# Optimization experiments

Hardware: AMD Instinct MI355X
Metric: run time of the kernel (lower is better)

The kernel has to match this reference:

```python
import jax, jax.numpy as jnp
import numpy as np

DIM, HEADS = 1024, 16
HEAD_DIM = DIM // HEADS
SCALE = HEAD_DIM ** -0.5


def setup_inputs() -> dict:
    key = jax.random.key(0)
    ks = jax.random.split(key, 5)
    B, N = 2, 2048
    x = jax.random.normal(ks[0], (B, N, DIM), dtype=jnp.float32)
    freqs = jax.random.normal(ks[1], (N, HEAD_DIM // 2), dtype=jnp.float32)
    w_qkv = jax.random.normal(ks[2], (3 * DIM, DIM), dtype=jnp.float32) * 0.02
    w_proj = jax.random.normal(ks[3], (DIM, DIM), dtype=jnp.float32) * 0.02
    b_proj = jnp.zeros((DIM,), dtype=jnp.float32)
    return {"x": x, "freqs": freqs, "w_qkv": w_qkv, "w_proj": w_proj, "b_proj": b_proj}


def _apply_rotary(t, cos, sin):
    # t: (B,N,H,D); cos/sin: (1,N,1,D//2)
    B, N, H, D = t.shape
    tp = t.reshape(B, N, H, D // 2, 2)
    x1, x2 = tp[..., 0], tp[..., 1]
    out = jnp.stack([x1 * cos - x2 * sin, x1 * sin + x2 * cos], axis=-1)
    return out.reshape(B, N, H, D)


def reference(x, freqs, w_qkv, w_proj, b_proj):
    B, N, C = x.shape
    H, D = HEADS, HEAD_DIM
    qkv = (x @ w_qkv.T).reshape(B, N, 3, H, D)  # fused QKV projection
    q, k, v = qkv[:, :, 0], qkv[:, :, 1], qkv[:, :, 2]  # each (B,N,H,D)
    cos = jnp.cos(freqs)[None, :, None, :]  # (1,N,1,D/2)
    sin = jnp.sin(freqs)[None, :, None, :]
    q = _apply_rotary(q, cos, sin)
    k = _apply_rotary(k, cos, sin)
    # SDPA: scores (B,H,N,N)
    scores = jnp.einsum("bqhd,bkhd->bhqk", q, k) * SCALE
    attn = jax.nn.softmax(scores, axis=-1)
    out = jnp.einsum("bhqk,bkhd->bqhd", attn, v).reshape(B, N, C)
    return out @ w_proj.T + b_proj
```

## Files before the change

### kernel.cpp

```cpp
#include <hip/hip_runtime.h>
#include <hip/hip_bf16.h>
#include <stdint.h>

#define BATCH   2
#define SEQ     2048
#define CDIM    1024
#define NHEAD   16
#define HDIM    64
#define MROWS   (BATCH*SEQ)
#define QKVN    (3*CDIM)
#define QSCALE  0.18033688011112042f

typedef __hip_bfloat16 bf16;
using bf16x8 = __attribute__((ext_vector_type(8))) __bf16;
using f32x4  = __attribute__((ext_vector_type(4))) float;
using s16x4  = __attribute__((ext_vector_type(4))) short;

__device__ __forceinline__ void gld16(const void* g, void* l) {
    __builtin_amdgcn_global_load_lds(
        (__attribute__((address_space(1))) void*)(void*)(g),
        (__attribute__((address_space(3))) void*)(l),
        16, 0, 0);
}

__device__ __forceinline__ f32x4 mfma16x16x32(bf16x8 a, bf16x8 b, f32x4 c) {
    return __builtin_amdgcn_mfma_f32_16x16x32_bf16(a, b, c, 0, 0, 0);
}
__device__ __forceinline__ f32x4 mfma16x16x16(s16x4 a, s16x4 b, f32x4 c) {
    return __builtin_amdgcn_mfma_f32_16x16x16bf16_1k(a, b, c, 0, 0, 0);
}

__device__ __forceinline__ uint16_t bfbits(float v) {
    bf16 b = __float2bfloat16(v);
    return *(uint16_t*)&b;
}
__device__ __forceinline__ uint32_t pkbf(float a, float b) {
    uint32_t au = __builtin_bit_cast(uint32_t, a);
    uint32_t bu = __builtin_bit_cast(uint32_t, b);
    return ((au + 0x8000u) >> 16) | ((bu + 0x8000u) & 0xffff0000u);
}

#define NX_F4 ((size_t)MROWS*CDIM/4)
#define NQ_F4 ((size_t)QKVN*CDIM/4)
#define NP_F4 ((size_t)CDIM*CDIM/4)
#define NF_SC ((size_t)SEQ*32)

__global__ __launch_bounds__(256)
void cvt_kernel(const float* __restrict__ x, const float* __restrict__ wq,
                const float* __restrict__ wp, const float* __restrict__ freqs,
                bf16* __restrict__ xb, bf16* __restrict__ wqb,
                bf16* __restrict__ wpb, float2* __restrict__ csn) {
    size_t i4 = (size_t)blockIdx.x*256 + threadIdx.x;
    if (i4 < NX_F4 + NQ_F4 + NP_F4) {
        const float* src; bf16* dst; size_t off;
        if (i4 < NX_F4)           { src = x;  dst = xb;  off = i4; }
        else if (i4 < NX_F4+NQ_F4){ src = wq; dst = wqb; off = i4 - NX_F4; }
        else                      { src = wp; dst = wpb; off = i4 - NX_F4 - NQ_F4; }
        float4 v = ((const float4*)src)[off];
        bf16 o[4] = { __float2bfloat16(v.x), __float2bfloat16(v.y),
                      __float2bfloat16(v.z), __float2bfloat16(v.w) };
        *(uint64_t*)(dst + off*4) = *(const uint64_t*)o;
    } else if (i4 < NX_F4 + NQ_F4 + NP_F4 + NF_SC) {
        size_t k = i4 - (NX_F4 + NQ_F4 + NP_F4);
        float f = freqs[k];
        csn[k] = make_float2(cosf(f), sinf(f));
    }
}

__global__ __launch_bounds__(256)
void gemm_qkv_rope(const bf16* __restrict__ A, const bf16* __restrict__ Bw,
                   const float2* __restrict__ csn, bf16* __restrict__ Qr,
                   bf16* __restrict__ Kr, bf16* __restrict__ VG) {
    const int K = CDIM;
    __shared__ __align__(16) bf16 As[128*32];
    __shared__ __align__(16) bf16 Bs[128*32];

    const int bm = blockIdx.x, bn = blockIdx.y;
    const int tid  = threadIdx.x;
    const int lane = tid & 63;
    const int w    = tid >> 6;
    const int wm   = (w & 1) * 64;
    const int wn   = (w >> 1) * 64;
    const int quad = lane >> 4;
    const int l16  = lane & 15;

    const int c0 = tid, c1 = tid + 256;
    const size_t a_off0 = (size_t)(bm*128 + (c0 >> 2)) * K + (c0 & 3) * 8;
    const size_t a_off1 = (size_t)(bm*128 + (c1 >> 2)) * K + (c1 & 3) * 8;
    const size_t b_off0 = (size_t)(bn*128 + (c0 >> 2)) * K + (c0 & 3) * 8;
    const size_t b_off1 = (size_t)(bn*128 + (c1 >> 2)) * K + (c1 & 3) * 8;

    f32x4 acc[4][4] = {};

    for (int k0 = 0; k0 < K; k0 += 32) {
        __syncthreads();
        gld16(A + a_off0 + k0, &As[c0*8]);
        gld16(A + a_off1 + k0, &As[c1*8]);
        gld16(Bw + b_off0 + k0, &Bs[c0*8]);
        gld16(Bw + b_off1 + k0, &Bs[c1*8]);
        __syncthreads();

        bf16x8 af[4], bfv[4];
#pragma unroll
        for (int i = 0; i < 4; i++)
            af[i] = *(const bf16x8*)&As[(wm + i*16 + l16)*32 + quad*8];
#pragma unroll
        for (int i = 0; i < 4; i++)
            bfv[i] = *(const bf16x8*)&Bs[(wn + i*16 + l16)*32 + quad*8];
#pragma unroll
        for (int mi = 0; mi < 4; mi++)
#pragma unroll
            for (int ni = 0; ni < 4; ni++)
                acc[mi][ni] = mfma16x16x32(af[mi], bfv[ni], acc[mi][ni]);
    }

    const int region = bn >> 3;
    if (region < 2) {
        bf16* dst = region ? Kr : Qr;
        const float qs = region ? 1.0f : QSCALE;
        const int odd = l16 & 1;
#pragma unroll
        for (int mi = 0; mi < 4; mi++) {
#pragma unroll
            for (int ni = 0; ni < 4; ni++) {
                const int cq = (bn & 7)*128 + wn + ni*16 + l16;
                const int h = cq >> 6, d = cq & 63, fi = d >> 1;
#pragma unroll
                for (int r = 0; r < 4; r++) {
                    const int m = bm*128 + wm + mi*16 + quad*4 + r;
                    const int bb = m >> 11, n = m & 2047;
                    float own = acc[mi][ni][r];
                    float prt = __shfl_xor(own, 1);
                    float2 cs2 = csn[n*32 + fi];
                    float o = odd ? (prt*cs2.y + own*cs2.x)
                                  : (own*cs2.x - prt*cs2.y);
                    dst[((size_t)(bb*16 + h)*SEQ + n)*HDIM + d] =
                        __float2bfloat16(o * qs);
                }
            }
        }
    } else {
        const int bb  = (bm*128) >> 11, n0l = (bm*128) & 2047;
        const int h   = (bn - 16)*2 + (wn >> 6);
        bf16* vg = VG + (size_t)(bb*16 + h) * (SEQ*HDIM);
#pragma unroll
        for (int mi = 0; mi < 4; mi++) {
            const int tile = (n0l >> 6) + ((wm + mi*16) >> 6);
            const int j    = ((wm + mi*16) >> 4) & 3;
#pragma unroll
            for (int ni = 0; ni < 4; ni++) {
                uint2 pk;
                pk.x = (uint32_t)bfbits(acc[mi][ni][0]) |
                       ((uint32_t)bfbits(acc[mi][ni][1]) << 16);
                pk.y = (uint32_t)bfbits(acc[mi][ni][2]) |
                       ((uint32_t)bfbits(acc[mi][ni][3]) << 16);
                const int slot = (j*4 + ni)*64 + quad*16 + l16;
                *(uint2*)&vg[(size_t)tile*4096 + slot*4] = pk;
            }
        }
    }
}

__global__ __launch_bounds__(256)
void gemm_proj(const bf16* __restrict__ A, const bf16* __restrict__ Bw,
               const float* __restrict__ bias, float* __restrict__ C,
               int M, int N, int K) {
    __shared__ __align__(16) bf16 As[64*32];
    __shared__ __align__(16) bf16 Bs[128*32];

    const int bm = blockIdx.x, bn = blockIdx.y;
    const int tid  = threadIdx.x;
    const int lane = tid & 63;
    const int w    = tid >> 6;
    const int wm   = (w & 1) * 32;
    const int wn   = (w >> 1) * 64;
    const int quad = lane >> 4;
    const int l16  = lane & 15;

    const int ca = tid, cb0 = tid, cb1 = tid + 256;
    const size_t a_off  = (size_t)(bm*64  + (ca  >> 2)) * K + (ca  & 3) * 8;
    const size_t b_off0 = (size_t)(bn*128 + (cb0 >> 2)) * K + (cb0 & 3) * 8;
    const size_t b_off1 = (size_t)(bn*128 + (cb1 >> 2)) * K + (cb1 & 3) * 8;

    f32x4 acc[2][4] = {};

    for (int k0 = 0; k0 < K; k0 += 32) {
        __syncthreads();
        gld16(A + a_off + k0, &As[ca*8]);
        gld16(Bw + b_off0 + k0, &Bs[cb0*8]);
        gld16(Bw + b_off1 + k0, &Bs[cb1*8]);
        __syncthreads();

        bf16x8 af[2], bfv[4];
#pragma unroll
        for (int i = 0; i < 2; i++)
            af[i] = *(const bf16x8*)&As[(wm + i*16 + l16)*32 + quad*8];
#pragma unroll
        for (int i = 0; i < 4; i++)
            bfv[i] = *(const bf16x8*)&Bs[(wn + i*16 + l16)*32 + quad*8];
#pragma unroll
        for (int mi = 0; mi < 2; mi++)
#pragma unroll
            for (int ni = 0; ni < 4; ni++)
                acc[mi][ni] = mfma16x16x32(af[mi], bfv[ni], acc[mi][ni]);
    }

#pragma unroll
    for (int mi = 0; mi < 2; mi++) {
        const int r0 = bm*64 + wm + mi*16 + quad*4;
#pragma unroll
        for (int ni = 0; ni < 4; ni++) {
            const int c = bn*128 + wn + ni*16 + l16;
            const float bv = bias[c];
#pragma unroll
            for (int r = 0; r < 4; r++)
                C[(size_t)(r0 + r)*N + c] = acc[mi][ni][r] + bv;
        }
    }
}

__global__ __launch_bounds__(64)
void attn_kernel(const bf16* __restrict__ Qr, const bf16* __restrict__ Kr,
                 const bf16* __restrict__ VG, bf16* __restrict__ Ao) {
    const int blk = blockIdx.x;
    const int bh  = blk >> 5;
    const int b   = bh >> 4, h = bh & 15;
    const int q0  = (blk & 31) * 64;
    const int lane = threadIdx.x;
    const int quad = lane >> 4, l16 = lane & 15;
    const int swz  = l16 & 7;

    __shared__ __align__(16) bf16 Ks[2][64*64];
    __shared__ __align__(16) bf16 Vs[2][64*64];

    bf16x8 qf[4][2];
#pragma unroll
    for (int t = 0; t < 4; t++) {
        const int qrow = q0 + t*16 + l16;
        const bf16* qp = Qr + ((size_t)bh*SEQ + qrow)*HDIM + quad*8;
        qf[t][0] = *(const bf16x8*)(qp);
        qf[t][1] = *(const bf16x8*)(qp + 32);
    }

    const bf16* KrB = Kr + (size_t)bh*SEQ*HDIM;
    const bf16* VgB = VG + (size_t)bh*SEQ*HDIM;
    int koff[8];
#pragma unroll
    for (int k = 0; k < 8; k++) {
        int c = lane + 64*k;
        int r = c >> 3, g = (c & 7) ^ (r & 7);
        koff[k] = r*HDIM + g*8;
    }

    f32x4 acc[4][4] = {};
    float lsum[4] = {};

#pragma unroll
    for (int k = 0; k < 8; k++) {
        gld16(KrB + koff[k], &Ks[0][(lane + 64*k)*8]);
        gld16(VgB + (lane + 64*k)*8, &Vs[0][(lane + 64*k)*8]);
    }

    for (int it = 0; it < SEQ/64; ++it) {
        const int cur = it & 1, nxt = cur ^ 1;
        bf16x8 kfr[4][2];
#pragma unroll
        for (int j = 0; j < 4; j++) {
            const bf16* krow = &Ks[cur][(j*16 + l16)*64];
            kfr[j][0] = *(const bf16x8*)(krow + ((quad     ^ swz) * 8));
            kfr[j][1] = *(const bf16x8*)(krow + (((quad+4) ^ swz) * 8));
        }
        s16x4 vfr[16];
#pragma unroll
        for (int m = 0; m < 16; m++)
            vfr[m] = *(const s16x4*)&Vs[cur][(m*64 + lane)*4];

        if (it + 1 < SEQ/64) {
            const size_t o = (size_t)(it + 1) * 4096;
#pragma unroll
            for (int k = 0; k < 8; k++) {
                gld16(KrB + koff[k] + o, &Ks[nxt][(lane + 64*k)*8]);
                gld16(VgB + (lane + 64*k)*8 + o, &Vs[nxt][(lane + 64*k)*8]);
            }
        }

        s16x4 pf[4][4];
#pragma unroll
        for (int j = 0; j < 4; j++) {
#pragma unroll
            for (int t = 0; t < 4; t++) {
                f32x4 sv = {};
                sv = mfma16x16x32(kfr[j][0], qf[t][0], sv);
                sv = mfma16x16x32(kfr[j][1], qf[t][1], sv);
                float e0 = __builtin_amdgcn_exp2f(sv[0]);
                float e1 = __builtin_amdgcn_exp2f(sv[1]);
                float e2 = __builtin_amdgcn_exp2f(sv[2]);
                float e3 = __builtin_amdgcn_exp2f(sv[3]);
                lsum[t] += (e0 + e1) + (e2 + e3);
                union { uint32_t u[2]; s16x4 v; } pa;
                pa.u[0] = pkbf(e0, e1);
                pa.u[1] = pkbf(e2, e3);
                pf[t][j] = pa.v;
            }
        }

#pragma unroll
        for (int dt = 0; dt < 4; dt++) {
#pragma unroll
            for (int j = 0; j < 4; j++) {
                s16x4 vf = vfr[j*4 + dt];
#pragma unroll
                for (int t = 0; t < 4; t++)
                    acc[t][dt] = mfma16x16x16(pf[t][j], vf, acc[t][dt]);
            }
        }
    }

#pragma unroll
    for (int t = 0; t < 4; t++) {
        lsum[t] += __shfl_xor(lsum[t], 16, 64);
        lsum[t] += __shfl_xor(lsum[t], 32, 64);
    }
    float lt[4][4];
#pragma unroll
    for (int t = 0; t < 4; t++)
#pragma unroll
        for (int r = 0; r < 4; r++)
            lt[t][r] = __shfl(lsum[t], quad*20 + r, 64);

#pragma unroll
    for (int t = 0; t < 4; t++)
#pragma unroll
        for (int dt = 0; dt < 4; dt++)
#pragma unroll
            for (int r = 0; r < 4; r++) {
                int qr  = q0 + t*16 + quad*4 + r;
                int col = h*HDIM + dt*16 + l16;
                Ao[(size_t)(b*SEQ + qr)*CDIM + col] =
                    __float2bfloat16(acc[t][dt][r] / lt[t][r]);
            }
}

extern "C" void kernel_launch(void* const* d_in, const int* in_sizes, int n_in,
                              void* d_out, int out_size, void* d_ws, size_t ws_size,
                              hipStream_t stream) {
    const float* x      = (const float*)d_in[0];
    const float* freqs  = (const float*)d_in[1];
    const float* w_qkv  = (const float*)d_in[2];
    const float* w_proj = (const float*)d_in[3];
    const float* b_proj = (const float*)d_in[4];
    float* out = (float*)d_out;

    char* ws = (char*)d_ws;
    bf16*   xb    = (bf16*)ws;   ws += (size_t)MROWS * CDIM * sizeof(bf16);
    bf16*   wqkvb = (bf16*)ws;   ws += (size_t)QKVN * CDIM * sizeof(bf16);
    bf16*   wprojb= (bf16*)ws;   ws += (size_t)CDIM * CDIM * sizeof(bf16);
    float2* csn   = (float2*)ws; ws += (size_t)SEQ * 32 * sizeof(float2);
    bf16*   Qr    = (bf16*)ws;   ws += (size_t)BATCH*NHEAD*SEQ*HDIM*sizeof(bf16);
    bf16*   Kr    = (bf16*)ws;   ws += (size_t)BATCH*NHEAD*SEQ*HDIM*sizeof(bf16);
    bf16*   VG    = (bf16*)ws;   ws += (size_t)BATCH*NHEAD*SEQ*HDIM*sizeof(bf16);
    bf16*   Ao    = (bf16*)ws;

    {
        size_t nthr = NX_F4 + NQ_F4 + NP_F4 + NF_SC;
        cvt_kernel<<<dim3((nthr + 255) / 256), dim3(256), 0, stream>>>(
            x, w_qkv, w_proj, freqs, xb, wqkvb, wprojb, csn);
    }
    gemm_qkv_rope<<<dim3(MROWS/128, QKVN/128), dim3(256), 0, stream>>>(
        xb, wqkvb, csn, Qr, Kr, VG);
    attn_kernel<<<dim3(BATCH*NHEAD*(SEQ/64)), dim3(64), 0, stream>>>(
        Qr, Kr, VG, Ao);
    gemm_proj<<<dim3(MROWS/64, CDIM/128), dim3(256), 0, stream>>>(
        Ao, wprojb, b_proj, out, MROWS, CDIM, CDIM);
}
```

Measured before the change: 208.3 us.

## Share K/V LDS tiles across four waves per attention block

The attention kernel now runs 256-thread blocks that cover 256 queries instead of 64-thread blocks that cover 64. The four waves load each K/V tile together and share it in LDS, so each tile is fetched from global memory or L2 four times less often. The prefetch of the next tile moves to the top of the loop behind a __syncthreads, which adds a block-wide barrier every iteration. The grid shrinks to a quarter as many blocks, which lowers the scheduler's flexibility in spreading work across CUs.

New measurement: 215.0 us. 3.2% more time.

```diff
diff --git a/kernel.cpp b/kernel.cpp
--- a/kernel.cpp
+++ b/kernel.cpp
@@ -219,14 +219,15 @@
     }
 }
 
-__global__ __launch_bounds__(64)
+__global__ __launch_bounds__(256)
 void attn_kernel(const bf16* __restrict__ Qr, const bf16* __restrict__ Kr,
                  const bf16* __restrict__ VG, bf16* __restrict__ Ao) {
     const int blk = blockIdx.x;
-    const int bh  = blk >> 5;
+    const int bh  = blk >> 3;
     const int b   = bh >> 4, h = bh & 15;
-    const int q0  = (blk & 31) * 64;
-    const int lane = threadIdx.x;
+    const int q0  = (blk & 7) * 256;
+    const int tid = threadIdx.x;
+    const int w   = tid >> 6, lane = tid & 63;
     const int quad = lane >> 4, l16 = lane & 15;
     const int swz  = l16 & 7;
 
@@ -236,7 +237,7 @@
     bf16x8 qf[4][2];
 #pragma unroll
     for (int t = 0; t < 4; t++) {
-        const int qrow = q0 + t*16 + l16;
+        const int qrow = q0 + w*64 + t*16 + l16;
         const bf16* qp = Qr + ((size_t)bh*SEQ + qrow)*HDIM + quad*8;
         qf[t][0] = *(const bf16x8*)(qp);
         qf[t][1] = *(const bf16x8*)(qp + 32);
@@ -244,25 +245,31 @@
 
     const bf16* KrB = Kr + (size_t)bh*SEQ*HDIM;
     const bf16* VgB = VG + (size_t)bh*SEQ*HDIM;
-    int koff[8];
-#pragma unroll
-    for (int k = 0; k < 8; k++) {
-        int c = lane + 64*k;
-        int r = c >> 3, g = (c & 7) ^ (r & 7);
-        koff[k] = r*HDIM + g*8;
-    }
+    const int c0 = tid, c1 = tid + 256;
+    const int r0 = c0 >> 3, g0 = (c0 & 7) ^ (r0 & 7);
+    const int r1 = c1 >> 3, g1 = (c1 & 7) ^ (r1 & 7);
+    const int koff0 = r0*HDIM + g0*8;
+    const int koff1 = r1*HDIM + g1*8;
 
     f32x4 acc[4][4] = {};
     float lsum[4] = {};
 
-#pragma unroll
-    for (int k = 0; k < 8; k++) {
-        gld16(KrB + koff[k], &Ks[0][(lane + 64*k)*8]);
-        gld16(VgB + (lane + 64*k)*8, &Vs[0][(lane + 64*k)*8]);
-    }
+    gld16(KrB + koff0, &Ks[0][c0*8]);
+    gld16(KrB + koff1, &Ks[0][c1*8]);
+    gld16(VgB + c0*8, &Vs[0][c0*8]);
+    gld16(VgB + c1*8, &Vs[0][c1*8]);
 
     for (int it = 0; it < SEQ/64; ++it) {
         const int cur = it & 1, nxt = cur ^ 1;
+        __syncthreads();
+        if (it + 1 < SEQ/64) {
+            const size_t o = (size_t)(it + 1) * 4096;
+            gld16(KrB + koff0 + o, &Ks[nxt][c0*8]);
+            gld16(KrB + koff1 + o, &Ks[nxt][c1*8]);
+            gld16(VgB + c0*8 + o, &Vs[nxt][c0*8]);
+            gld16(VgB + c1*8 + o, &Vs[nxt][c1*8]);
+        }
+
         bf16x8 kfr[4][2];
 #pragma unroll
         for (int j = 0; j < 4; j++) {
@@ -274,15 +281,6 @@
 #pragma unroll
         for (int m = 0; m < 16; m++)
             vfr[m] = *(const s16x4*)&Vs[cur][(m*64 + lane)*4];
-
-        if (it + 1 < SEQ/64) {
-            const size_t o = (size_t)(it + 1) * 4096;
-#pragma unroll
-            for (int k = 0; k < 8; k++) {
-                gld16(KrB + koff[k] + o, &Ks[nxt][(lane + 64*k)*8]);
-                gld16(VgB + (lane + 64*k)*8 + o, &Vs[nxt][(lane + 64*k)*8]);
-            }
-        }
 
         s16x4 pf[4][4];
 #pragma unroll
@@ -334,7 +332,7 @@
         for (int dt = 0; dt < 4; dt++)
 #pragma unroll
             for (int r = 0; r < 4; r++) {
-                int qr  = q0 + t*16 + quad*4 + r;
+                int qr  = q0 + w*64 + t*16 + quad*4 + r;
                 int col = h*HDIM + dt*16 + l16;
                 Ao[(size_t)(b*SEQ + qr)*CDIM + col] =
                     __float2bfloat16(acc[t][dt][r] / lt[t][r]);
@@ -368,7 +366,7 @@
     }
     gemm_qkv_rope<<<dim3(MROWS/128, QKVN/128), dim3(256), 0, stream>>>(
         xb, wqkvb, csn, Qr, Kr, VG);
-    attn_kernel<<<dim3(BATCH*NHEAD*(SEQ/64)), dim3(64), 0, stream>>>(
+    attn_kernel<<<dim3(BATCH*NHEAD*(SEQ/256)), dim3(256), 0, stream>>>(
         Qr, Kr, VG, Ao);
     gemm_proj<<<dim3(MROWS/64, CDIM/128), dim3(256), 0, stream>>>(
         Ao, wprojb, b_proj, out, MROWS, CDIM, CDIM);
```
